# Kernel tuning notes

Hardware: AMD Instinct MI355X
Metric: run time of the kernel (lower is better)

The kernel has to match this reference:

```python
import jax, jax.numpy as jnp
import numpy as np

N = 100000
IN_C, HID_C, OUT_C = 128, 128, 128
E = 3200000


def gcn_conv(x, src, dst, W, b, num_nodes):
    # Linear transform first (smaller feature dim already), then normalized scatter-add.
    h = x @ W  # [N, out]
    # symmetric normalization with self-loops already included in (src, dst)
    deg = jax.ops.segment_sum(jnp.ones_like(dst, dtype=h.dtype), dst, num_segments=num_nodes)
    dinv = jnp.where(deg > 0, jax.lax.rsqrt(deg), 0.0)  # deg^{-1/2}
    norm = dinv[src] * dinv[dst]  # [E_total]
    msgs = h[src] * norm[:, None]  # gather + scale, [E_total, out]
    out = jax.ops.segment_sum(msgs, dst, num_segments=num_nodes)  # scatter-add
    return out + b


def add_self_loops(edge_index, num_nodes):
    loop = jnp.arange(num_nodes, dtype=edge_index.dtype)
    src = jnp.concatenate([edge_index[0], loop])
    dst = jnp.concatenate([edge_index[1], loop])
    return src, dst


def setup_inputs() -> dict:
    key = jax.random.key(0)
    k1, k2, k3, k4, k5 = jax.random.split(key, 5)
    x = jax.random.normal(k1, (N, IN_C), dtype=jnp.float32)
    edge_index = jax.random.randint(k2, (2, E), 0, N, dtype=jnp.int64)
    # Glorot-ish init for GCN weights
    W1 = jax.random.normal(k3, (IN_C, HID_C), dtype=jnp.float32) * (1.0 / np.sqrt(IN_C))
    b1 = jnp.zeros((HID_C,), dtype=jnp.float32)
    W2 = jax.random.normal(k4, (HID_C, OUT_C), dtype=jnp.float32) * (1.0 / np.sqrt(HID_C))
    b2 = jnp.zeros((OUT_C,), dtype=jnp.float32)
    return {"x": x, "edge_index": edge_index, "W1": W1, "b1": b1, "W2": W2, "b2": b2}


def reference(x, edge_index, W1, b1, W2, b2):
    src, dst = add_self_loops(edge_index, N)
    h = gcn_conv(x, src, dst, W1, b1, N)
    h = jax.nn.relu(h)
    out = gcn_conv(h, src, dst, W2, b2, N)
    return out
```

## Files before the change

kernel.cpp:

```cpp
#include <hip/hip_runtime.h>


#define NPB 128
#define NBMAX 1024
#define EPT 64
#define PART_TILE (256 * EPT)

typedef unsigned short ushort_t;
typedef __attribute__((ext_vector_type(8))) short short8;
typedef __attribute__((ext_vector_type(4))) float f32x4;

__device__ __forceinline__ unsigned short f32_to_bf16_rne(float x) {
    unsigned int v = __float_as_uint(x);
    unsigned int r = v + 0x7fffu + ((v >> 16) & 1u);
    return (unsigned short)(r >> 16);
}

__global__ __launch_bounds__(256) void k_wprep(
    const float* __restrict__ W1, const float* __restrict__ W2,
    ushort_t* __restrict__ Wp1, ushort_t* __restrict__ Wp2) {
    int idx = blockIdx.x * 256 + threadIdx.x;
    int which = idx >> 14;
    int e = idx & 16383;
    int n = e & 127, k = e >> 7;
    const float* W = which ? W2 : W1;
    ushort_t* Wp = which ? Wp2 : Wp1;
    Wp[n * 128 + k] = f32_to_bf16_rne(W[k * 128 + n]);
}

__global__ __launch_bounds__(256) void k_hist_tiles(
    const int* __restrict__ dst, int* __restrict__ C,
    int e, int nbp, int total) {
    __shared__ int hist[NBMAX];
    int t = threadIdx.x;
    int tile = blockIdx.x;
    for (int k = t; k < nbp; k += 256) hist[k] = 0;
    __syncthreads();
    int t0 = tile * PART_TILE;
#pragma unroll 4
    for (int j = 0; j < EPT; j++) {
        int i = t0 + j * 256 + t;
        if (i < total) {
            int d = (i < e) ? dst[i] : (i - e);
            atomicAdd(&hist[d >> 7], 1);
        }
    }
    __syncthreads();
    int* row = C + (size_t)tile * nbp;
    for (int k = t; k < nbp; k += 256) row[k] = hist[k];
}

__global__ __launch_bounds__(256) void k_col_scan(
    int* __restrict__ C, int* __restrict__ colsum, int T, int nbp) {
    int b = blockIdx.x * 256 + threadIdx.x;
    if (b >= nbp) return;
    int running = 0;
    int t = 0;
    for (; t + 8 <= T; t += 8) {
        int v[8];
#pragma unroll
        for (int j = 0; j < 8; j++) v[j] = C[(size_t)(t + j) * nbp + b];
#pragma unroll
        for (int j = 0; j < 8; j++) {
            C[(size_t)(t + j) * nbp + b] = running;
            running += v[j];
        }
    }
    for (; t < T; t++) {
        int v = C[(size_t)t * nbp + b];
        C[(size_t)t * nbp + b] = running;
        running += v;
    }
    colsum[b] = running;
}

__global__ __launch_bounds__(256) void k_bucket_scan(
    const int* __restrict__ colsum, int* __restrict__ bucket_ptr,
    int nbp, int total) {
    __shared__ int sd[256];
    int t = threadIdx.x;
    int c[4];
#pragma unroll
    for (int j = 0; j < 4; j++) {
        int k = t * 4 + j;
        c[j] = (k < nbp) ? colsum[k] : 0;
    }
    int s = c[0] + c[1] + c[2] + c[3];
    sd[t] = s;
    __syncthreads();
    for (int off = 1; off < 256; off <<= 1) {
        int v = (t >= off) ? sd[t - off] : 0;
        __syncthreads();
        sd[t] += v;
        __syncthreads();
    }
    int pre = sd[t] - s;
#pragma unroll
    for (int j = 0; j < 4; j++) {
        int k = t * 4 + j;
        if (k < nbp) bucket_ptr[k] = pre;
        pre += c[j];
    }
    if (t == 255) bucket_ptr[nbp] = total;
}

__global__ __launch_bounds__(256) void k_partition(
    const int* __restrict__ src, const int* __restrict__ dst,
    const int* __restrict__ C, const int* __restrict__ bucket_ptr,
    unsigned int* __restrict__ pairs, int e, int nbp, int total) {
    __shared__ int lcur[NBMAX];
    int t = threadIdx.x;
    int tile = blockIdx.x;
    const int* row = C + (size_t)tile * nbp;
    for (int k = t; k < nbp; k += 256) lcur[k] = row[k] + bucket_ptr[k];
    __syncthreads();
    int t0 = tile * PART_TILE;
#pragma unroll 4
    for (int j = 0; j < EPT; j++) {
        int i = t0 + j * 256 + t;
        if (i < total) {
            int s, d;
            if (i < e) { s = src[i]; d = dst[i]; }
            else       { s = i - e;  d = s; }
            int b = d >> 7;
            int off = atomicAdd(&lcur[b], 1);
            pairs[off] = (unsigned int)s | ((unsigned int)(d & 127) << 17);
        }
    }
}

__global__ __launch_bounds__(256) void k_build(
    const unsigned int* __restrict__ pairs, const int* __restrict__ bucket_ptr,
    int* __restrict__ row_ptr, int* __restrict__ srcs,
    float* __restrict__ dinv, int n) {
    __shared__ int cnt[NPB];
    __shared__ int scn[NPB];
    __shared__ int cur[NPB];
    int b = blockIdx.x;
    int t = threadIdx.x;
    int node0 = b << 7;
    int p0 = bucket_ptr[b], p1 = bucket_ptr[b + 1];
    if (t < NPB) cnt[t] = 0;
    __syncthreads();
    for (int i = p0 + t; i < p1; i += 256) {
        int dlow = (int)(pairs[i] >> 17) & 127;
        atomicAdd(&cnt[dlow], 1);
    }
    __syncthreads();
    if (t < NPB) scn[t] = cnt[t];
    __syncthreads();
    for (int off = 1; off < NPB; off <<= 1) {
        int v = (t < NPB && t >= off) ? scn[t - off] : 0;
        __syncthreads();
        if (t < NPB) scn[t] += v;
        __syncthreads();
    }
    if (t < NPB) {
        int incl = scn[t];
        int excl = incl - cnt[t];
        int start = p0 + excl;
        cur[t] = start;
        int node = node0 + t;
        if (node < n) {
            row_ptr[node] = start;
            dinv[node] = rsqrtf((float)cnt[t]);
            if (node == n - 1) row_ptr[n] = p0 + incl;
        }
    }
    __syncthreads();
    for (int i = p0 + t; i < p1; i += 256) {
        unsigned int pr = pairs[i];
        int pos = atomicAdd(&cur[(pr >> 17) & 127], 1);
        srcs[pos] = (int)(pr & 0x1FFFFu);
    }
}

__global__ __launch_bounds__(256) void k_gemm1(
    const float* __restrict__ A, const ushort_t* __restrict__ Wp,
    const float* __restrict__ dinv, ushort_t* __restrict__ G, int M) {
    int t = threadIdx.x;
    int row0 = blockIdx.x * 64;
    int wv = t >> 6;
    int lane = t & 63;
    int m = lane & 15;
    int quad = lane >> 4;

    int gr_row = row0 + wv * 16 + m;
    int gcl = gr_row < M ? gr_row : M - 1;
    const float* ap = A + (size_t)gcl * 128 + quad * 8;

    f32x4 acc[8];
#pragma unroll
    for (int c = 0; c < 8; c++) acc[c] = (f32x4){0.f, 0.f, 0.f, 0.f};

#pragma unroll
    for (int ks = 0; ks < 4; ks++) {
        int kb = ks * 32 + quad * 8;
        float xs[8];
        *(float4*)&xs[0] = *(const float4*)(ap + ks * 32);
        *(float4*)&xs[4] = *(const float4*)(ap + ks * 32 + 4);
        short8 ahi, alo;
#pragma unroll
        for (int j = 0; j < 8; j++) {
            unsigned short h = f32_to_bf16_rne(xs[j]);
            ahi[j] = (short)h;
            float hf = __uint_as_float((unsigned int)h << 16);
            alo[j] = (short)f32_to_bf16_rne(xs[j] - hf);
        }
#pragma unroll
        for (int c = 0; c < 8; c++) {
            short8 b8 = *(const short8*)(Wp + (size_t)(c * 16 + m) * 128 + kb);
            acc[c] = __builtin_amdgcn_mfma_f32_16x16x32_bf16(ahi, b8, acc[c], 0, 0, 0);
            acc[c] = __builtin_amdgcn_mfma_f32_16x16x32_bf16(alo, b8, acc[c], 0, 0, 0);
        }
    }

    int rbase = row0 + wv * 16 + quad * 4;
#pragma unroll
    for (int reg = 0; reg < 4; reg++) {
        int gr = rbase + reg;
        if (gr < M) {
            float dv = dinv[gr];
#pragma unroll
            for (int c = 0; c < 8; c++)
                G[(size_t)gr * 128 + c * 16 + m] = f32_to_bf16_rne(acc[c][reg] * dv);
        }
    }
}

__global__ __launch_bounds__(256) void k_gemm2(
    ushort_t* actG2, const ushort_t* __restrict__ Wp,
    const float* __restrict__ dinv, int M) {
    int t = threadIdx.x;
    int row0 = blockIdx.x * 64;
    int wv = t >> 6;
    int lane = t & 63;
    int m = lane & 15;
    int quad = lane >> 4;

    int gr_row = row0 + wv * 16 + m;
    int gcl = gr_row < M ? gr_row : M - 1;
    const ushort_t* ap = actG2 + (size_t)gcl * 128;

    f32x4 acc[8];
#pragma unroll
    for (int c = 0; c < 8; c++) acc[c] = (f32x4){0.f, 0.f, 0.f, 0.f};

#pragma unroll
    for (int ks = 0; ks < 4; ks++) {
        int kb = ks * 32 + quad * 8;
        short8 a8 = *(const short8*)(ap + kb);
#pragma unroll
        for (int c = 0; c < 8; c++) {
            short8 b8 = *(const short8*)(Wp + (size_t)(c * 16 + m) * 128 + kb);
            acc[c] = __builtin_amdgcn_mfma_f32_16x16x32_bf16(a8, b8, acc[c], 0, 0, 0);
        }
    }

    int rbase = row0 + wv * 16 + quad * 4;
#pragma unroll
    for (int reg = 0; reg < 4; reg++) {
        int gr = rbase + reg;
        if (gr < M) {
            float dv = dinv[gr];
#pragma unroll
            for (int c = 0; c < 8; c++)
                actG2[(size_t)gr * 128 + c * 16 + m] = f32_to_bf16_rne(acc[c][reg] * dv);
        }
    }
}

__global__ __launch_bounds__(256) void k_agg1(
    const int* __restrict__ row_ptr, const int* __restrict__ srcs,
    const ushort_t* __restrict__ G, const float* __restrict__ dinv,
    const float* __restrict__ bias, unsigned int* __restrict__ ActOut, int n) {
    int wid = (blockIdx.x * 256 + threadIdx.x) >> 6;
    int lane = threadIdx.x & 63;
    if (wid >= n) return;
    int beg = row_ptr[wid], end = row_ptr[wid + 1];
    int c = lane * 2;
    float a0 = 0.f, a1 = 0.f;
    int p = beg;
    for (; p + 8 <= end; p += 8) {
        unsigned int u[8];
#pragma unroll
        for (int j = 0; j < 8; j++) {
            int s = srcs[p + j];
            u[j] = *(const unsigned int*)(G + (size_t)s * 128 + c);
        }
#pragma unroll
        for (int j = 0; j < 8; j++) {
            a0 += __uint_as_float(u[j] << 16);
            a1 += __uint_as_float(u[j] & 0xffff0000u);
        }
    }
    for (; p + 4 <= end; p += 4) {
        unsigned int u[4];
#pragma unroll
        for (int j = 0; j < 4; j++) {
            int s = srcs[p + j];
            u[j] = *(const unsigned int*)(G + (size_t)s * 128 + c);
        }
#pragma unroll
        for (int j = 0; j < 4; j++) {
            a0 += __uint_as_float(u[j] << 16);
            a1 += __uint_as_float(u[j] & 0xffff0000u);
        }
    }
    for (; p < end; p++) {
        int s = srcs[p];
        unsigned int u = *(const unsigned int*)(G + (size_t)s * 128 + c);
        a0 += __uint_as_float(u << 16);
        a1 += __uint_as_float(u & 0xffff0000u);
    }
    float dv = dinv[wid];
    a0 = fmaxf(fmaf(a0, dv, bias[c]), 0.f);
    a1 = fmaxf(fmaf(a1, dv, bias[c + 1]), 0.f);
    unsigned int uo = (unsigned int)f32_to_bf16_rne(a0) |
                      ((unsigned int)f32_to_bf16_rne(a1) << 16);
    ActOut[(size_t)wid * 64 + lane] = uo;
}

__global__ __launch_bounds__(256) void k_agg2(
    const int* __restrict__ row_ptr, const int* __restrict__ srcs,
    const ushort_t* __restrict__ G, const float* __restrict__ dinv,
    const float* __restrict__ bias, float* __restrict__ Out, int n) {
    int wid = (blockIdx.x * 256 + threadIdx.x) >> 6;
    int lane = threadIdx.x & 63;
    if (wid >= n) return;
    int beg = row_ptr[wid], end = row_ptr[wid + 1];
    int c = lane * 2;
    float a0 = 0.f, a1 = 0.f;
    int p = beg;
    for (; p + 8 <= end; p += 8) {
        unsigned int u[8];
#pragma unroll
        for (int j = 0; j < 8; j++) {
            int s = srcs[p + j];
            u[j] = *(const unsigned int*)(G + (size_t)s * 128 + c);
        }
#pragma unroll
        for (int j = 0; j < 8; j++) {
            a0 += __uint_as_float(u[j] << 16);
            a1 += __uint_as_float(u[j] & 0xffff0000u);
        }
    }
    for (; p + 4 <= end; p += 4) {
        unsigned int u[4];
#pragma unroll
        for (int j = 0; j < 4; j++) {
            int s = srcs[p + j];
            u[j] = *(const unsigned int*)(G + (size_t)s * 128 + c);
        }
#pragma unroll
        for (int j = 0; j < 4; j++) {
            a0 += __uint_as_float(u[j] << 16);
            a1 += __uint_as_float(u[j] & 0xffff0000u);
        }
    }
    for (; p < end; p++) {
        int s = srcs[p];
        unsigned int u = *(const unsigned int*)(G + (size_t)s * 128 + c);
        a0 += __uint_as_float(u << 16);
        a1 += __uint_as_float(u & 0xffff0000u);
    }
    float dv = dinv[wid];
    a0 = fmaf(a0, dv, bias[c]);
    a1 = fmaf(a1, dv, bias[c + 1]);
    unsigned long long uv = ((unsigned long long)__float_as_uint(a1) << 32) |
                            (unsigned long long)__float_as_uint(a0);
    __builtin_nontemporal_store(uv, (unsigned long long*)(Out + (size_t)wid * 128 + c));
}

extern "C" void kernel_launch(void* const* d_in, const int* in_sizes, int n_in,
                              void* d_out, int out_size, void* d_ws, size_t ws_size,
                              hipStream_t stream) {
    const float* x  = (const float*)d_in[0];
    const int*   ei = (const int*)d_in[1];
    const float* W1 = (const float*)d_in[2];
    const float* b1 = (const float*)d_in[3];
    const float* W2 = (const float*)d_in[4];
    const float* b2 = (const float*)d_in[5];
    float* out = (float*)d_out;

    const int C = 128;
    const int N = in_sizes[0] / C;
    const int E = in_sizes[1] / 2;
    const int* src = ei;
    const int* dst = ei + E;
    const int total = E + N;
    const int nbp = (N + NPB - 1) >> 7;
    const int T = (total + PART_TILE - 1) / PART_TILE;

    char* ws = (char*)d_ws;
    size_t off = 0;
    auto alloc = [&](size_t bytes) -> void* {
        void* p = ws + off;
        off = (off + bytes + 511) & ~(size_t)511;
        return p;
    };
    int*   Cmat       = (int*)alloc((size_t)T * nbp * 4);
    int*   colsum     = (int*)alloc((size_t)nbp * 4);
    int*   bucket_ptr = (int*)alloc((size_t)(nbp + 1) * 4);
    int*   row_ptr    = (int*)alloc(((size_t)N + 1) * 4);
    float* dinv       = (float*)alloc((size_t)N * 4);
    int*   srcs       = (int*)alloc((size_t)total * 4);
    ushort_t* Wp1     = (ushort_t*)alloc(128 * 128 * 2);
    ushort_t* Wp2     = (ushort_t*)alloc(128 * 128 * 2);
    ushort_t* G1      = (ushort_t*)alloc((size_t)N * C * 2);
    size_t ab = (size_t)N * C * 2, pb = (size_t)total * 4;
    void* shared = alloc(ab > pb ? ab : pb);
    ushort_t* actG2 = (ushort_t*)shared;
    unsigned int* pairs = (unsigned int*)shared;

    k_wprep<<<128, 256, 0, stream>>>(W1, W2, Wp1, Wp2);
    k_hist_tiles<<<T, 256, 0, stream>>>(dst, Cmat, E, nbp, total);
    k_col_scan<<<(nbp + 255) / 256, 256, 0, stream>>>(Cmat, colsum, T, nbp);
    k_bucket_scan<<<1, 256, 0, stream>>>(colsum, bucket_ptr, nbp, total);
    k_partition<<<T, 256, 0, stream>>>(src, dst, Cmat, bucket_ptr, pairs, E, nbp, total);
    k_build<<<nbp, 256, 0, stream>>>(pairs, bucket_ptr, row_ptr, srcs, dinv, N);

    k_gemm1<<<(N + 63) / 64, 256, 0, stream>>>(x, Wp1, dinv, G1, N);
    k_agg1<<<(N + 3) / 4, 256, 0, stream>>>(row_ptr, srcs, G1, dinv, b1,
                                            (unsigned int*)actG2, N);

    k_gemm2<<<(N + 63) / 64, 256, 0, stream>>>(actG2, Wp2, dinv, N);
    k_agg2<<<(N + 3) / 4, 256, 0, stream>>>(row_ptr, srcs, actG2, dinv, b2, out, N);
}
```

Before: 519.0 us.

## Store features in column-chunked layout and split aggregation into per-chunk passes

The GEMM outputs are now written in a layout of 8 column chunks of 16 bf16 each, so each chunk of the node table is a contiguous 3.2MB slab. Aggregation launches a 2D grid with one chunk per grid row. Each wave processes 16 edges at a time, reading 32-byte pieces, and finishes with a shuffle reduction. The intent is to make each chunk's gather working set fit in cache and raise cache hit rates on random gathers. In exchange, srcs and row_ptr are read 8 times and there is extra shuffle-reduction work, and partial-wave masking wastes lanes on low-degree nodes.

```diff
diff --git a/kernel.cpp b/kernel.cpp
--- a/kernel.cpp
+++ b/kernel.cpp
@@ -5,8 +5,10 @@
 #define NBMAX 1024
 #define EPT 64
 #define PART_TILE (256 * EPT)
+#define NCHUNK 8
 
 typedef unsigned short ushort_t;
+typedef unsigned long long ull_t;
 typedef __attribute__((ext_vector_type(8))) short short8;
 typedef __attribute__((ext_vector_type(4))) float f32x4;
 
@@ -223,7 +225,7 @@
             float dv = dinv[gr];
 #pragma unroll
             for (int c = 0; c < 8; c++)
-                G[(size_t)gr * 128 + c * 16 + m] = f32_to_bf16_rne(acc[c][reg] * dv);
+                G[((size_t)c * M + gr) * 16 + m] = f32_to_bf16_rne(acc[c][reg] * dv);
         }
     }
 }
@@ -240,7 +242,6 @@
 
     int gr_row = row0 + wv * 16 + m;
     int gcl = gr_row < M ? gr_row : M - 1;
-    const ushort_t* ap = actG2 + (size_t)gcl * 128;
 
     f32x4 acc[8];
 #pragma unroll
@@ -249,7 +250,7 @@
 #pragma unroll
     for (int ks = 0; ks < 4; ks++) {
         int kb = ks * 32 + quad * 8;
-        short8 a8 = *(const short8*)(ap + kb);
+        short8 a8 = *(const short8*)(actG2 + ((size_t)(kb >> 4) * M + gcl) * 16 + (kb & 15));
 #pragma unroll
         for (int c = 0; c < 8; c++) {
             short8 b8 = *(const short8*)(Wp + (size_t)(c * 16 + m) * 128 + kb);
@@ -265,111 +266,115 @@
             float dv = dinv[gr];
 #pragma unroll
             for (int c = 0; c < 8; c++)
-                actG2[(size_t)gr * 128 + c * 16 + m] = f32_to_bf16_rne(acc[c][reg] * dv);
-        }
-    }
-}
+                actG2[((size_t)c * M + gr) * 16 + m] = f32_to_bf16_rne(acc[c][reg] * dv);
+        }
+    }
+}
+
 
 __global__ __launch_bounds__(256) void k_agg1(
     const int* __restrict__ row_ptr, const int* __restrict__ srcs,
     const ushort_t* __restrict__ G, const float* __restrict__ dinv,
-    const float* __restrict__ bias, unsigned int* __restrict__ ActOut, int n) {
+    const float* __restrict__ bias, ull_t* __restrict__ ActOut, int n) {
+    int chunk = blockIdx.y;
     int wid = (blockIdx.x * 256 + threadIdx.x) >> 6;
     int lane = threadIdx.x & 63;
     if (wid >= n) return;
     int beg = row_ptr[wid], end = row_ptr[wid + 1];
-    int c = lane * 2;
-    float a0 = 0.f, a1 = 0.f;
-    int p = beg;
-    for (; p + 8 <= end; p += 8) {
-        unsigned int u[8];
-#pragma unroll
-        for (int j = 0; j < 8; j++) {
-            int s = srcs[p + j];
-            u[j] = *(const unsigned int*)(G + (size_t)s * 128 + c);
-        }
-#pragma unroll
-        for (int j = 0; j < 8; j++) {
-            a0 += __uint_as_float(u[j] << 16);
-            a1 += __uint_as_float(u[j] & 0xffff0000u);
-        }
-    }
-    for (; p + 4 <= end; p += 4) {
-        unsigned int u[4];
-#pragma unroll
-        for (int j = 0; j < 4; j++) {
-            int s = srcs[p + j];
-            u[j] = *(const unsigned int*)(G + (size_t)s * 128 + c);
-        }
-#pragma unroll
-        for (int j = 0; j < 4; j++) {
-            a0 += __uint_as_float(u[j] << 16);
-            a1 += __uint_as_float(u[j] & 0xffff0000u);
-        }
-    }
-    for (; p < end; p++) {
-        int s = srcs[p];
-        unsigned int u = *(const unsigned int*)(G + (size_t)s * 128 + c);
-        a0 += __uint_as_float(u << 16);
-        a1 += __uint_as_float(u & 0xffff0000u);
-    }
-    float dv = dinv[wid];
-    a0 = fmaxf(fmaf(a0, dv, bias[c]), 0.f);
-    a1 = fmaxf(fmaf(a1, dv, bias[c + 1]), 0.f);
-    unsigned int uo = (unsigned int)f32_to_bf16_rne(a0) |
-                      ((unsigned int)f32_to_bf16_rne(a1) << 16);
-    ActOut[(size_t)wid * 64 + lane] = uo;
+    int g = lane >> 2;
+    int q = lane & 3;
+    const ull_t* T = (const ull_t*)(G + (size_t)chunk * n * 16);
+    float a0 = 0.f, a1 = 0.f, a2 = 0.f, a3 = 0.f;
+    for (int p = beg; p < end; p += 32) {
+#pragma unroll
+        for (int j = 0; j < 2; j++) {
+            int g0 = p + j * 16;
+            if (g0 < end) {
+                int eidx = g0 + g;
+                bool ok = eidx < end;
+                int s = srcs[ok ? eidx : end - 1];
+                ull_t u = T[(size_t)s * 4 + q];
+                if (!ok) u = 0ull;
+                unsigned int u0 = (unsigned int)u, u1 = (unsigned int)(u >> 32);
+                a0 += __uint_as_float(u0 << 16);
+                a1 += __uint_as_float(u0 & 0xffff0000u);
+                a2 += __uint_as_float(u1 << 16);
+                a3 += __uint_as_float(u1 & 0xffff0000u);
+            }
+        }
+    }
+#pragma unroll
+    for (int off = 4; off < 64; off <<= 1) {
+        a0 += __shfl_xor(a0, off);
+        a1 += __shfl_xor(a1, off);
+        a2 += __shfl_xor(a2, off);
+        a3 += __shfl_xor(a3, off);
+    }
+    if (g == 0) {
+        float dv = dinv[wid];
+        const float* bp = bias + chunk * 16 + q * 4;
+        a0 = fmaxf(fmaf(a0, dv, bp[0]), 0.f);
+        a1 = fmaxf(fmaf(a1, dv, bp[1]), 0.f);
+        a2 = fmaxf(fmaf(a2, dv, bp[2]), 0.f);
+        a3 = fmaxf(fmaf(a3, dv, bp[3]), 0.f);
+        unsigned int p0 = (unsigned int)f32_to_bf16_rne(a0) |
+                          ((unsigned int)f32_to_bf16_rne(a1) << 16);
+        unsigned int p1 = (unsigned int)f32_to_bf16_rne(a2) |
+                          ((unsigned int)f32_to_bf16_rne(a3) << 16);
+        ull_t uo = (ull_t)p0 | ((ull_t)p1 << 32);
+        __builtin_nontemporal_store(uo, ActOut + ((size_t)chunk * n + wid) * 4 + q);
+    }
 }
 
 __global__ __launch_bounds__(256) void k_agg2(
     const int* __restrict__ row_ptr, const int* __restrict__ srcs,
     const ushort_t* __restrict__ G, const float* __restrict__ dinv,
     const float* __restrict__ bias, float* __restrict__ Out, int n) {
+    int chunk = blockIdx.y;
     int wid = (blockIdx.x * 256 + threadIdx.x) >> 6;
     int lane = threadIdx.x & 63;
     if (wid >= n) return;
     int beg = row_ptr[wid], end = row_ptr[wid + 1];
-    int c = lane * 2;
-    float a0 = 0.f, a1 = 0.f;
-    int p = beg;
-    for (; p + 8 <= end; p += 8) {
-        unsigned int u[8];
-#pragma unroll
-        for (int j = 0; j < 8; j++) {
-            int s = srcs[p + j];
-            u[j] = *(const unsigned int*)(G + (size_t)s * 128 + c);
-        }
-#pragma unroll
-        for (int j = 0; j < 8; j++) {
-            a0 += __uint_as_float(u[j] << 16);
-            a1 += __uint_as_float(u[j] & 0xffff0000u);
-        }
-    }
-    for (; p + 4 <= end; p += 4) {
-        unsigned int u[4];
-#pragma unroll
-        for (int j = 0; j < 4; j++) {
-            int s = srcs[p + j];
-            u[j] = *(const unsigned int*)(G + (size_t)s * 128 + c);
-        }
-#pragma unroll
-        for (int j = 0; j < 4; j++) {
-            a0 += __uint_as_float(u[j] << 16);
-            a1 += __uint_as_float(u[j] & 0xffff0000u);
-        }
-    }
-    for (; p < end; p++) {
-        int s = srcs[p];
-        unsigned int u = *(const unsigned int*)(G + (size_t)s * 128 + c);
-        a0 += __uint_as_float(u << 16);
-        a1 += __uint_as_float(u & 0xffff0000u);
-    }
-    float dv = dinv[wid];
-    a0 = fmaf(a0, dv, bias[c]);
-    a1 = fmaf(a1, dv, bias[c + 1]);
-    unsigned long long uv = ((unsigned long long)__float_as_uint(a1) << 32) |
-                            (unsigned long long)__float_as_uint(a0);
-    __builtin_nontemporal_store(uv, (unsigned long long*)(Out + (size_t)wid * 128 + c));
+    int g = lane >> 2;
+    int q = lane & 3;
+    const ull_t* T = (const ull_t*)(G + (size_t)chunk * n * 16);
+    float a0 = 0.f, a1 = 0.f, a2 = 0.f, a3 = 0.f;
+    for (int p = beg; p < end; p += 32) {
+#pragma unroll
+        for (int j = 0; j < 2; j++) {
+            int g0 = p + j * 16;
+            if (g0 < end) {
+                int eidx = g0 + g;
+                bool ok = eidx < end;
+                int s = srcs[ok ? eidx : end - 1];
+                ull_t u = T[(size_t)s * 4 + q];
+                if (!ok) u = 0ull;
+                unsigned int u0 = (unsigned int)u, u1 = (unsigned int)(u >> 32);
+                a0 += __uint_as_float(u0 << 16);
+                a1 += __uint_as_float(u0 & 0xffff0000u);
+                a2 += __uint_as_float(u1 << 16);
+                a3 += __uint_as_float(u1 & 0xffff0000u);
+            }
+        }
+    }
+#pragma unroll
+    for (int off = 4; off < 64; off <<= 1) {
+        a0 += __shfl_xor(a0, off);
+        a1 += __shfl_xor(a1, off);
+        a2 += __shfl_xor(a2, off);
+        a3 += __shfl_xor(a3, off);
+    }
+    if (g == 0) {
+        float dv = dinv[wid];
+        const float* bp = bias + chunk * 16 + q * 4;
+        f32x4 o;
+        o.x = fmaf(a0, dv, bp[0]);
+        o.y = fmaf(a1, dv, bp[1]);
+        o.z = fmaf(a2, dv, bp[2]);
+        o.w = fmaf(a3, dv, bp[3]);
+        __builtin_nontemporal_store(o,
+            (f32x4*)(Out + (size_t)wid * 128 + chunk * 16 + q * 4));
+    }
 }
 
 extern "C" void kernel_launch(void* const* d_in, const int* in_sizes, int n_in,
@@ -420,10 +425,13 @@
     k_partition<<<T, 256, 0, stream>>>(src, dst, Cmat, bucket_ptr, pairs, E, nbp, total);
     k_build<<<nbp, 256, 0, stream>>>(pairs, bucket_ptr, row_ptr, srcs, dinv, N);
 
+    const int NB = (N + 3) / 4;
+    dim3 agrid(NB, NCHUNK);
+
     k_gemm1<<<(N + 63) / 64, 256, 0, stream>>>(x, Wp1, dinv, G1, N);
-    k_agg1<<<(N + 3) / 4, 256, 0, stream>>>(row_ptr, srcs, G1, dinv, b1,
-                                            (unsigned int*)actG2, N);
+    k_agg1<<<agrid, 256, 0, stream>>>(row_ptr, srcs, G1, dinv, b1,
+                                      (ull_t*)actG2, N);
 
     k_gemm2<<<(N + 63) / 64, 256, 0, stream>>>(actG2, Wp2, dinv, N);
-    k_agg2<<<(N + 3) / 4, 256, 0, stream>>>(row_ptr, srcs, actG2, dinv, b2, out, N);
-}
+    k_agg2<<<agrid, 256, 0, stream>>>(row_ptr, srcs, actG2, dinv, b2, out, N);
+}
```

Result: slower. 884.8 us (+70.5%).
